# Performance work log

Measured on AMD Instinct MI355X. Metric: run time of the kernel, lower is better.

Reference implementation:

```python
import jax, jax.numpy as jnp
import numpy as np

D = 1024
H = 16
HD = D // H
SCALE = HD ** -0.5
EPS = 1e-5

def _ln(x, g, b):
    m = jnp.mean(x, axis=-1, keepdims=True)
    v = jnp.mean((x - m) ** 2, axis=-1, keepdims=True)
    return (x - m) / jnp.sqrt(v + EPS) * g + b

def setup_inputs() -> dict:
    key = jax.random.key(0)
    ks = jax.random.split(key, 16)
    B, Lq, Lk = 8, 1024, 1024
    s = 0.02
    inp = {
        "q": jax.random.normal(ks[0], (B, Lq, D), jnp.float32),
        "kv": jax.random.normal(ks[1], (B, Lk, D), jnp.float32),
        "kv_mask": jax.random.randint(ks[2], (B, Lk), 0, 2).astype(bool),
        "Wq": jax.random.normal(ks[3], (D, D), jnp.float32) * s,
        "bq": jnp.zeros((D,), jnp.float32),
        "Wk": jax.random.normal(ks[4], (D, D), jnp.float32) * s,
        "bk": jnp.zeros((D,), jnp.float32),
        "Wv": jax.random.normal(ks[5], (D, D), jnp.float32) * s,
        "bv": jnp.zeros((D,), jnp.float32),
        "Wo": jax.random.normal(ks[6], (D, D), jnp.float32) * s,
        "bo": jnp.zeros((D,), jnp.float32),
        "ln1_g": jnp.ones((D,), jnp.float32),
        "ln1_b": jnp.zeros((D,), jnp.float32),
        "W1": jax.random.normal(ks[7], (D, 4 * D), jnp.float32) * s,
        "b1": jnp.zeros((4 * D,), jnp.float32),
        "W2": jax.random.normal(ks[8], (4 * D, D), jnp.float32) * s,
        "b2": jnp.zeros((D,), jnp.float32),
        "ln2_g": jnp.ones((D,), jnp.float32),
        "ln2_b": jnp.zeros((D,), jnp.float32),
    }
    return inp

def reference(q, kv, kv_mask, Wq, bq, Wk, bk, Wv, bv, Wo, bo, ln1_g, ln1_b, W1, b1, W2, b2, ln2_g, ln2_b):
    B, Lq, _ = q.shape
    Lk = kv.shape[1]
    # projections -> [B, H, L, HD]
    qp = (q @ Wq + bq).reshape(B, Lq, H, HD).transpose(0, 2, 1, 3)
    kp = (kv @ Wk + bk).reshape(B, Lk, H, HD).transpose(0, 2, 1, 3)
    vp = (kv @ Wv + bv).reshape(B, Lk, H, HD).transpose(0, 2, 1, 3)
    scores = jnp.einsum('bhqd,bhkd->bhqk', qp, kp) * SCALE
    # mask: True = pad; if a row is all-pad, un-mask the last key position
    all_pad = jnp.all(kv_mask, axis=1)  # [B]
    mask = kv_mask.at[:, -1].set(jnp.where(all_pad, False, kv_mask[:, -1]))
    scores = jnp.where(mask[:, None, None, :], jnp.float32(-10000.0), scores)
    attn = jax.nn.softmax(scores, axis=-1)  # dropout is identity at eval
    out = jnp.einsum('bhqk,bhkd->bhqd', attn, vp)
    out = out.transpose(0, 2, 1, 3).reshape(B, Lq, D)
    out = out @ Wo + bo
    x = _ln(q + out, ln1_g, ln1_b)
    x2 = jax.nn.relu(x @ W1 + b1) @ W2 + b2
    return _ln(x + x2, ln2_g, ln2_b)
```

## Files before the change

### kernel.cpp

```cpp
#include <hip/hip_runtime.h>

typedef __bf16 bf16_t;
typedef bf16_t bf16x8 __attribute__((ext_vector_type(8)));
typedef bf16_t bf16x4 __attribute__((ext_vector_type(4)));
typedef float f32x4 __attribute__((ext_vector_type(4)));
typedef unsigned int u32;

typedef __attribute__((address_space(1))) unsigned as1_u32;
typedef __attribute__((address_space(3))) unsigned as3_u32;

#define LOG2E 1.4426950408889634f
#define QSCALE (0.125f * LOG2E)
#define MASK2 (-10000.0f * LOG2E)

__device__ __forceinline__ void gload16(const void* g, void* l) {
  __builtin_amdgcn_global_load_lds((as1_u32*)(void*)g, (as3_u32*)l, 16, 0, 0);
}

__global__ void cvt_qkv(const float* __restrict__ q, const float* __restrict__ kv,
                        bf16_t* __restrict__ qb, bf16_t* __restrict__ kvb) {
  long i = ((long)blockIdx.x * 256 + threadIdx.x) * 8;
  const float* src; bf16_t* dst;
  if (i < 8388608) { src = q + i; dst = qb + i; }
  else { src = kv + (i - 8388608); dst = kvb + (i - 8388608); }
  const float4 a = *(const float4*)src;
  const float4 b = *(const float4*)(src + 4);
  bf16x8 o;
  o[0] = (bf16_t)a.x; o[1] = (bf16_t)a.y; o[2] = (bf16_t)a.z; o[3] = (bf16_t)a.w;
  o[4] = (bf16_t)b.x; o[5] = (bf16_t)b.y; o[6] = (bf16_t)b.z; o[7] = (bf16_t)b.w;
  *(bf16x8*)dst = o;
}

__global__ void prep_mask(const unsigned char* __restrict__ mraw,
                          float* __restrict__ maskf) {
  __shared__ int sred[256];
  const int t = threadIdx.x, b = blockIdx.x;
  int f = 0;
  for (int i = t; i < 2048; i += 256) {
    u32 v = ((const u32*)mraw)[i];
    if (v & 0xFFFFFF00u) f = 1;
  }
  sred[t] = f; __syncthreads();
  for (int s = 128; s; s >>= 1) { if (t < s) sred[t] |= sred[t + s]; __syncthreads(); }
  const int isByte = sred[0];
  __syncthreads();

  int vals[4]; int allpad = 1;
#pragma unroll
  for (int i = 0; i < 4; i++) {
    int k = t * 4 + i;
    int mv = isByte ? (int)mraw[b * 1024 + k] : ((const int*)mraw)[b * 1024 + k];
    vals[i] = (mv != 0);
    allpad &= vals[i];
  }
  sred[t] = allpad; __syncthreads();
  for (int s = 128; s; s >>= 1) { if (t < s) sred[t] &= sred[t + s]; __syncthreads(); }
  const int ap = sred[0];
#pragma unroll
  for (int i = 0; i < 4; i++) {
    int k = t * 4 + i;
    int m = vals[i];
    if (ap && k == 1023) m = 0;
    maskf[b * 1024 + k] = m ? MASK2 : 0.0f;
  }
}

struct TP { const float* s; bf16_t* d; int K; int N; };
struct TP6 { TP t[6]; };
__global__ void transpose_all(TP6 args) {
  __shared__ float tile[64][65];
  int bid = blockIdx.x, z, tx, ty;
  if (bid < 1024)      { z = bid >> 8;  int r = bid & 255;  tx = r & 15; ty = r >> 4; }
  else if (bid < 2048) { z = 4;         int r = bid - 1024; tx = r & 63; ty = r >> 6; }
  else                 { z = 5;         int r = bid - 2048; tx = r & 15; ty = r >> 4; }
  const TP a = args.t[z];
  const int t = threadIdx.x;
  const int n0 = tx * 64, k0 = ty * 64;
#pragma unroll
  for (int i = 0; i < 16; i++) {
    int e = i * 256 + t; int r = e >> 6, c = e & 63;
    tile[r][c] = a.s[(size_t)(k0 + r) * a.N + n0 + c];
  }
  __syncthreads();
#pragma unroll
  for (int i = 0; i < 16; i++) {
    int e = i * 256 + t; int r = e >> 6, c = e & 63;
    a.d[(size_t)(n0 + r) * a.K + k0 + c] = (bf16_t)tile[c][r];
  }
}

template<int BM, int BN, int NT>
__global__ __launch_bounds__(NT, 2)
void gemm_bt(const bf16_t* __restrict__ A, const bf16_t* __restrict__ BT,
             const float* __restrict__ bias, bf16_t* __restrict__ C,
             int M, int N, int K, int relu, int bias_mode, float scale) {
  constexpr int WAVES = NT / 64;
  constexpr int WNC = (BN == 256) ? 4 : 2;
  constexpr int WMC = WAVES / WNC;
  constexpr int M_REP = BM / (WMC * 16);
  constexpr int N_REP = BN / (WNC * 16);
  constexpr int JA = BM * 8 / NT;
  constexpr int JB = BN * 8 / NT;

  __shared__ __align__(16) bf16_t As[2][BM * 64];
  __shared__ __align__(16) bf16_t Bs[2][BN * 64];

  const int tid = threadIdx.x;
  const int wave = tid >> 6, lane = tid & 63;
  const int quad = lane >> 4, l15 = lane & 15;
  const int gx = gridDim.x;
  const int nwg = gx * gridDim.y;
  int lin = blockIdx.y * gx + blockIdx.x;
  lin = (lin & 7) * (nwg >> 3) + (lin >> 3);
  const long bm = (long)(lin / gx) * BM, bn = (long)(lin % gx) * BN;
  const int wm = (wave / WNC) * (M_REP * 16), wn = (wave % WNC) * (N_REP * 16);

  const bf16_t* agp[JA];
  const bf16_t* bgp[JB];
#pragma unroll
  for (int j = 0; j < JA; j++) {
    int e = j * NT + tid, r = e >> 3, c = (e & 7) ^ (r & 7);
    agp[j] = A + (bm + r) * (long)K + c * 8;
  }
#pragma unroll
  for (int j = 0; j < JB; j++) {
    int e = j * NT + tid, r = e >> 3, c = (e & 7) ^ (r & 7);
    bgp[j] = BT + (bn + r) * (long)K + c * 8;
  }

  int aoff[M_REP][2], boff[N_REP][2];
#pragma unroll
  for (int mi = 0; mi < M_REP; mi++)
#pragma unroll
    for (int ks = 0; ks < 2; ks++) {
      int row = wm + mi * 16 + l15;
      aoff[mi][ks] = row * 64 + (((ks * 4 + quad) ^ (row & 7)) * 8);
    }
#pragma unroll
  for (int ni = 0; ni < N_REP; ni++)
#pragma unroll
    for (int ks = 0; ks < 2; ks++) {
      int row = wn + ni * 16 + l15;
      boff[ni][ks] = row * 64 + (((ks * 4 + quad) ^ (row & 7)) * 8);
    }

  f32x4 acc[M_REP][N_REP];
#pragma unroll
  for (int i = 0; i < M_REP; i++)
#pragma unroll
    for (int j = 0; j < N_REP; j++) acc[i][j] = (f32x4){0.f, 0.f, 0.f, 0.f};

  auto stage = [&](int kt, int s) {
#pragma unroll
    for (int j = 0; j < JA; j++)
      gload16(agp[j] + (long)kt * 64, &As[s][(j * NT + wave * 64) * 8]);
#pragma unroll
    for (int j = 0; j < JB; j++)
      gload16(bgp[j] + (long)kt * 64, &Bs[s][(j * NT + wave * 64) * 8]);
  };

  const int T = K >> 6;
  stage(0, 0);
  for (int t = 0; t < T; t++) {
    const int s = t & 1;
    if (t + 1 < T) {
      stage(t + 1, s ^ 1);
      asm volatile("s_waitcnt vmcnt(8)" ::: "memory");
    } else {
      asm volatile("s_waitcnt vmcnt(0)" ::: "memory");
    }
    __builtin_amdgcn_s_barrier();

#pragma unroll
    for (int ks = 0; ks < 2; ks++) {
      bf16x8 af[M_REP], bf[N_REP];
#pragma unroll
      for (int mi = 0; mi < M_REP; mi++) af[mi] = *(const bf16x8*)&As[s][aoff[mi][ks]];
#pragma unroll
      for (int ni = 0; ni < N_REP; ni++) bf[ni] = *(const bf16x8*)&Bs[s][boff[ni][ks]];
      __builtin_amdgcn_s_setprio(1);
#pragma unroll
      for (int mi = 0; mi < M_REP; mi++)
#pragma unroll
        for (int ni = 0; ni < N_REP; ni++)
          acc[mi][ni] = __builtin_amdgcn_mfma_f32_16x16x32_bf16(af[mi], bf[ni], acc[mi][ni], 0, 0, 0);
      __builtin_amdgcn_s_setprio(0);
    }
    asm volatile("s_waitcnt lgkmcnt(0)" ::: "memory");
    __builtin_amdgcn_s_barrier();
  }

#pragma unroll
  for (int mi = 0; mi < M_REP; mi++) {
#pragma unroll
    for (int ni = 0; ni < N_REP; ni++) {
      const long col = bn + wn + ni * 16 + l15;
      const float bc = bias_mode ? 0.f : bias[col];
#pragma unroll
      for (int r = 0; r < 4; r++) {
        const long row = bm + wm + mi * 16 + quad * 4 + r;
        const float bb = bias_mode ? bias[row] : bc;
        float v = (acc[mi][ni][r] + bb) * scale;
        if (relu) v = v > 0.f ? v : 0.f;
        C[row * N + col] = (bf16_t)v;
      }
    }
  }
}

__global__ __launch_bounds__(256, 4)
void attn(const bf16_t* __restrict__ Q, const bf16_t* __restrict__ Kp,
          const bf16_t* __restrict__ Vt, const float* __restrict__ maskf,
          bf16_t* __restrict__ AO) {
  __shared__ __align__(16) bf16_t Qs[64 * 64];
  __shared__ __align__(16) bf16_t Ks[64 * 64];
  __shared__ __align__(16) bf16_t Vts[64 * 64];
  __shared__ __align__(16) bf16_t Ps[4][16 * 64];
  __shared__ __align__(16) float msk[64];

  const int tid = threadIdx.x;
  const int wave = tid >> 6, lane = tid & 63;
  const int quad = lane >> 4, l15 = lane & 15;
  int lin = (blockIdx.z * 16 + blockIdx.y) * 16 + blockIdx.x;
  lin = (lin & 7) * 256 + (lin >> 3);
  const int q0 = (lin & 15) * 64;
  const int h = (lin >> 4) & 15;
  const int b = lin >> 8;

  const long base_q = ((long)b * 1024 + q0) * 1024 + h * 64;
  const long base_k = (long)b * 1024 * 1024 + h * 64;
  const long base_v = (long)h * 64 * 8192 + b * 1024;

  const int r0 = tid >> 3;
  const int c0 = ((tid & 7) ^ (r0 & 7)) * 8;
  const int r1 = (256 + tid) >> 3;
  const int c1 = (((256 + tid) & 7) ^ (r1 & 7)) * 8;
  const int wd0 = wave * 64 * 8;
  const int wd1 = (256 + wave * 64) * 8;

  const bf16_t* qg0 = Q + base_q + (long)r0 * 1024 + c0;
  const bf16_t* qg1 = Q + base_q + (long)r1 * 1024 + c1;
  const bf16_t* kg0 = Kp + base_k + (long)r0 * 1024 + c0;
  const bf16_t* kg1 = Kp + base_k + (long)r1 * 1024 + c1;
  const bf16_t* vg0 = Vt + base_v + (long)r0 * 8192 + c0;
  const bf16_t* vg1 = Vt + base_v + (long)r1 * 8192 + c1;
  const float* mrow = maskf + b * 1024;

  gload16(qg0, &Qs[wd0]);
  gload16(qg1, &Qs[wd1]);

  int offKV[4][2], offP[2], pwOff[4];
#pragma unroll
  for (int nt = 0; nt < 4; nt++)
#pragma unroll
    for (int ks = 0; ks < 2; ks++)
      offKV[nt][ks] = (nt * 16 + l15) * 64 + (((ks * 4 + quad) ^ (l15 & 7)) * 8);
#pragma unroll
  for (int ks = 0; ks < 2; ks++)
    offP[ks] = l15 * 64 + (((ks * 4 + quad) ^ (l15 & 7)) * 8);
#pragma unroll
  for (int nt = 0; nt < 4; nt++)
    pwOff[nt] = l15 * 64 + (((nt * 2 + (quad >> 1)) ^ (l15 & 7)) * 8) + (quad & 1) * 4;

  __syncthreads();

  bf16x8 aq[2];
#pragma unroll
  for (int ks = 0; ks < 2; ks++) {
    const int row = wave * 16 + l15;
    aq[ks] = *(const bf16x8*)&Qs[row * 64 + (((ks * 4 + quad) ^ (row & 7)) * 8)];
  }

  float m_i = -1e30f, l_i = 0.f;
  f32x4 o[4];
#pragma unroll
  for (int nt = 0; nt < 4; nt++) o[nt] = (f32x4){0.f, 0.f, 0.f, 0.f};

  bf16_t* Pw = &Ps[wave][0];

  for (int kt = 0; kt < 16; kt++) {
    const int k0 = kt * 64;
    __syncthreads();
    gload16(kg0 + (long)k0 * 1024, &Ks[wd0]);
    gload16(kg1 + (long)k0 * 1024, &Ks[wd1]);
    gload16(vg0 + k0, &Vts[wd0]);
    gload16(vg1 + k0, &Vts[wd1]);
    if (tid < 64) msk[tid] = mrow[k0 + tid];
    __syncthreads();

    f32x4 mv[4];
#pragma unroll
    for (int nt = 0; nt < 4; nt++)
      mv[nt] = *(const f32x4*)&msk[nt * 16 + quad * 4];

    f32x4 sc[4];
#pragma unroll
    for (int nt = 0; nt < 4; nt++) {
      f32x4 s = mv[nt];
#pragma unroll
      for (int ks = 0; ks < 2; ks++) {
        bf16x8 bk = *(const bf16x8*)&Ks[offKV[nt][ks]];
        s = __builtin_amdgcn_mfma_f32_16x16x32_bf16(bk, aq[ks], s, 0, 0, 0);
      }
      sc[nt] = s;
    }

    float mx = -1e30f;
#pragma unroll
    for (int nt = 0; nt < 4; nt++)
#pragma unroll
      for (int r = 0; r < 4; r++) mx = fmaxf(mx, sc[nt][r]);
    mx = fmaxf(mx, __shfl_xor(mx, 16));
    mx = fmaxf(mx, __shfl_xor(mx, 32));
    const float mnew = fmaxf(m_i, mx);
    const float alpha = exp2f(m_i - mnew);
    m_i = mnew;
    float ps = 0.f;
#pragma unroll
    for (int nt = 0; nt < 4; nt++)
#pragma unroll
      for (int r = 0; r < 4; r++) {
        const float p = exp2f(sc[nt][r] - mnew);
        sc[nt][r] = p;
        ps += p;
      }
    ps += __shfl_xor(ps, 16);
    ps += __shfl_xor(ps, 32);
    l_i = l_i * alpha + ps;

    float a4[4];
#pragma unroll
    for (int r = 0; r < 4; r++)
      a4[r] = __shfl(alpha, (quad << 4) | (quad * 4 + r));
#pragma unroll
    for (int nt = 0; nt < 4; nt++)
#pragma unroll
      for (int r = 0; r < 4; r++) o[nt][r] *= a4[r];

#pragma unroll
    for (int nt = 0; nt < 4; nt++) {
      bf16x4 pv;
#pragma unroll
      for (int r = 0; r < 4; r++) pv[r] = (bf16_t)sc[nt][r];
      *(bf16x4*)&Pw[pwOff[nt]] = pv;
    }

#pragma unroll
    for (int ks = 0; ks < 2; ks++) {
      bf16x8 ap = *(const bf16x8*)&Pw[offP[ks]];
#pragma unroll
      for (int nt = 0; nt < 4; nt++) {
        bf16x8 bv = *(const bf16x8*)&Vts[offKV[nt][ks]];
        o[nt] = __builtin_amdgcn_mfma_f32_16x16x32_bf16(ap, bv, o[nt], 0, 0, 0);
      }
    }
  }

  float linv[4];
#pragma unroll
  for (int r = 0; r < 4; r++)
    linv[r] = 1.0f / __shfl(l_i, (quad << 4) | (quad * 4 + r));
#pragma unroll
  for (int r = 0; r < 4; r++) {
    const int row = q0 + wave * 16 + quad * 4 + r;
#pragma unroll
    for (int nt = 0; nt < 4; nt++) {
      const int col = h * 64 + nt * 16 + l15;
      AO[((long)b * 1024 + row) * 1024 + col] = (bf16_t)(o[nt][r] * linv[r]);
    }
  }
}

__global__ __launch_bounds__(256)
void ln_res1(const float* __restrict__ xa, const bf16_t* __restrict__ xb,
             const float* __restrict__ g, const float* __restrict__ bt,
             bf16_t* __restrict__ out) {
  __shared__ float sw[8];
  const int t = threadIdx.x, w = t >> 6;
  const long row = blockIdx.x;
  const float4 a = *(const float4*)(xa + row * 1024 + t * 4);
  const bf16x4 bq = *(const bf16x4*)(xb + row * 1024 + t * 4);
  float v[4] = {a.x + (float)bq[0], a.y + (float)bq[1],
                a.z + (float)bq[2], a.w + (float)bq[3]};
  float s = v[0] + v[1] + v[2] + v[3];
  float s2 = v[0]*v[0] + v[1]*v[1] + v[2]*v[2] + v[3]*v[3];
#pragma unroll
  for (int off = 1; off < 64; off <<= 1) {
    s += __shfl_xor(s, off); s2 += __shfl_xor(s2, off);
  }
  if ((t & 63) == 0) { sw[w] = s; sw[4 + w] = s2; }
  __syncthreads();
  s = sw[0] + sw[1] + sw[2] + sw[3];
  s2 = sw[4] + sw[5] + sw[6] + sw[7];
  const float mean = s * (1.f / 1024.f);
  const float var = s2 * (1.f / 1024.f) - mean * mean;
  const float rstd = rsqrtf(var + 1e-5f);
  bf16x4 o;
#pragma unroll
  for (int i = 0; i < 4; i++) {
    const int c = t * 4 + i;
    o[i] = (bf16_t)((v[i] - mean) * rstd * g[c] + bt[c]);
  }
  *(bf16x4*)(out + row * 1024 + t * 4) = o;
}

__global__ __launch_bounds__(256)
void ln_res2(const bf16_t* __restrict__ xa, const bf16_t* __restrict__ xb,
             const float* __restrict__ g, const float* __restrict__ bt,
             float* __restrict__ out) {
  __shared__ float sw[8];
  const int t = threadIdx.x, w = t >> 6;
  const long row = blockIdx.x;
  const bf16x4 aq = *(const bf16x4*)(xa + row * 1024 + t * 4);
  const bf16x4 bq = *(const bf16x4*)(xb + row * 1024 + t * 4);
  float v[4];
#pragma unroll
  for (int i = 0; i < 4; i++) v[i] = (float)aq[i] + (float)bq[i];
  float s = v[0] + v[1] + v[2] + v[3];
  float s2 = v[0]*v[0] + v[1]*v[1] + v[2]*v[2] + v[3]*v[3];
#pragma unroll
  for (int off = 1; off < 64; off <<= 1) {
    s += __shfl_xor(s, off); s2 += __shfl_xor(s2, off);
  }
  if ((t & 63) == 0) { sw[w] = s; sw[4 + w] = s2; }
  __syncthreads();
  s = sw[0] + sw[1] + sw[2] + sw[3];
  s2 = sw[4] + sw[5] + sw[6] + sw[7];
  const float mean = s * (1.f / 1024.f);
  const float var = s2 * (1.f / 1024.f) - mean * mean;
  const float rstd = rsqrtf(var + 1e-5f);
  float4 o;
  o.x = (v[0] - mean) * rstd * g[t*4+0] + bt[t*4+0];
  o.y = (v[1] - mean) * rstd * g[t*4+1] + bt[t*4+1];
  o.z = (v[2] - mean) * rstd * g[t*4+2] + bt[t*4+2];
  o.w = (v[3] - mean) * rstd * g[t*4+3] + bt[t*4+3];
  *(float4*)(out + row * 1024 + t * 4) = o;
}

extern "C" void kernel_launch(void* const* d_in, const int* in_sizes, int n_in,
                              void* d_out, int out_size, void* d_ws, size_t ws_size,
                              hipStream_t stream) {
  (void)in_sizes; (void)n_in; (void)out_size; (void)ws_size;
  const float* q   = (const float*)d_in[0];
  const float* kv  = (const float*)d_in[1];
  const unsigned char* mraw = (const unsigned char*)d_in[2];
  const float* Wq = (const float*)d_in[3];
  const float* bq = (const float*)d_in[4];
  const float* Wk = (const float*)d_in[5];
  const float* bk = (const float*)d_in[6];
  const float* Wv = (const float*)d_in[7];
  const float* bv = (const float*)d_in[8];
  const float* Wo = (const float*)d_in[9];
  const float* bo = (const float*)d_in[10];
  const float* g1 = (const float*)d_in[11];
  const float* be1 = (const float*)d_in[12];
  const float* W1 = (const float*)d_in[13];
  const float* b1 = (const float*)d_in[14];
  const float* W2 = (const float*)d_in[15];
  const float* b2 = (const float*)d_in[16];
  const float* g2 = (const float*)d_in[17];
  const float* be2 = (const float*)d_in[18];
  float* out = (float*)d_out;

  char* ws = (char*)d_ws;
  size_t off = 0;
  auto alloc = [&](size_t bytes) -> char* {
    char* p = ws + off; off += (bytes + 255) & ~(size_t)255; return p;
  };
  const size_t MB16 = (size_t)8192 * 1024 * 2;
  float*  maskf = (float*)alloc(8192 * 4);
  bf16_t* WqT = (bf16_t*)alloc((size_t)1024 * 1024 * 2);
  bf16_t* WkT = (bf16_t*)alloc((size_t)1024 * 1024 * 2);
  bf16_t* WvT = (bf16_t*)alloc((size_t)1024 * 1024 * 2);
  bf16_t* WoT = (bf16_t*)alloc((size_t)1024 * 1024 * 2);
  bf16_t* W1T = (bf16_t*)alloc((size_t)1024 * 4096 * 2);
  bf16_t* W2T = (bf16_t*)alloc((size_t)4096 * 1024 * 2);
  bf16_t* Qp = (bf16_t*)alloc(MB16);
  bf16_t* Kp = (bf16_t*)alloc(MB16);
  bf16_t* VT = (bf16_t*)alloc(MB16);
  bf16_t* AO = (bf16_t*)alloc(MB16);
  bf16_t* X1 = (bf16_t*)alloc(MB16);
  bf16_t* TL = (bf16_t*)alloc(MB16);
  bf16_t* qb  = X1;
  bf16_t* kvb = TL;
  bf16_t* HF  = Qp;
  bf16_t* OP  = Kp;
  bf16_t* F2  = WqT;

  cvt_qkv<<<8192, 256, 0, stream>>>(q, kv, qb, kvb);
  prep_mask<<<8, 256, 0, stream>>>(mraw, maskf);
  TP6 tp = {{ {Wq, WqT, 1024, 1024}, {Wk, WkT, 1024, 1024},
              {Wv, WvT, 1024, 1024}, {Wo, WoT, 1024, 1024},
              {W1, W1T, 1024, 4096}, {W2, W2T, 4096, 1024} }};
  transpose_all<<<3072, 256, 0, stream>>>(tp);

  const dim3 gproj(8, 64);
  gemm_bt<128,128,256><<<gproj, 256, 0, stream>>>(qb,  WqT, bq, Qp, 8192, 1024, 1024, 0, 0, QSCALE);
  gemm_bt<128,128,256><<<gproj, 256, 0, stream>>>(kvb, WkT, bk, Kp, 8192, 1024, 1024, 0, 0, 1.f);
  gemm_bt<128,128,256><<<dim3(64, 8), 256, 0, stream>>>(WvT, kvb, bv, VT, 1024, 8192, 1024, 0, 1, 1.f);

  attn<<<dim3(16, 16, 8), 256, 0, stream>>>(Qp, Kp, VT, maskf, AO);

  gemm_bt<128,128,256><<<gproj, 256, 0, stream>>>(AO, WoT, bo, OP, 8192, 1024, 1024, 0, 0, 1.f);
  ln_res1<<<8192, 256, 0, stream>>>(q, OP, g1, be1, X1);

  gemm_bt<256,256,512><<<dim3(16, 32), 512, 0, stream>>>(X1, W1T, b1, HF, 8192, 4096, 1024, 1, 0, 1.f);
  gemm_bt<128,128,256><<<gproj, 256, 0, stream>>>(HF, W2T, b2, F2, 8192, 1024, 4096, 0, 0, 1.f);
  ln_res2<<<8192, 256, 0, stream>>>(X1, F2, g2, be2, out);
}
```

Measured before the change: 556.7 us.

## Add ping-pong pipelined 256x256 GEMM kernel for the FFN up-projection

Adds a dedicated 512-thread GEMM kernel for the W1 projection. It uses double-buffered LDS with global_load_lds and issues the next tile's loads in four chunks interleaved between MFMA phases, with barriers and s_setprio to overlap memory with compute. It also remaps workgroup IDs across groups of eight for better L2 locality and uses XOR-swizzled LDS offsets. The extra barriers and the large accumulator register footprint at 8x4 tiles per wave could limit occupancy.

Result: no change. 549.9 us (-1.2%).

```diff
diff --git a/kernel.cpp b/kernel.cpp
--- a/kernel.cpp
+++ b/kernel.cpp
@@ -201,6 +201,118 @@
         const long row = bm + wm + mi * 16 + quad * 4 + r;
         const float bb = bias_mode ? bias[row] : bc;
         float v = (acc[mi][ni][r] + bb) * scale;
+        if (relu) v = v > 0.f ? v : 0.f;
+        C[row * N + col] = (bf16_t)v;
+      }
+    }
+  }
+}
+
+__global__ __launch_bounds__(512, 2)
+void gemm_8p(const bf16_t* __restrict__ A, const bf16_t* __restrict__ BT,
+             const float* __restrict__ bias, bf16_t* __restrict__ C,
+             int M, int N, int K, int relu, float scale) {
+  __shared__ __align__(16) bf16_t As[2][256 * 64];
+  __shared__ __align__(16) bf16_t Bs[2][256 * 64];
+
+  const int tid = threadIdx.x;
+  const int wave = tid >> 6, lane = tid & 63;
+  const int quad = lane >> 4, l15 = lane & 15;
+  const int gx = gridDim.x;
+  const int nwg = gx * gridDim.y;
+  int lin = blockIdx.y * gx + blockIdx.x;
+  lin = (lin & 7) * (nwg >> 3) + (lin >> 3);
+  const long bm = (long)(lin / gx) * 256, bn = (long)(lin % gx) * 256;
+  const int wm = (wave >> 2) * 128, wn = (wave & 3) * 64;
+
+  const int r_ = tid >> 3;
+  const int cs_ = ((tid & 7) ^ (r_ & 7)) * 8;
+  const bf16_t* ag = A + (bm + r_) * (long)K + cs_;
+  const bf16_t* bg = BT + (bn + r_) * (long)K + cs_;
+
+  int aoff[8][2], boff[4][2];
+#pragma unroll
+  for (int mi = 0; mi < 8; mi++)
+#pragma unroll
+    for (int ks = 0; ks < 2; ks++) {
+      int row = wm + mi * 16 + l15;
+      aoff[mi][ks] = row * 64 + (((ks * 4 + quad) ^ (row & 7)) * 8);
+    }
+#pragma unroll
+  for (int ni = 0; ni < 4; ni++)
+#pragma unroll
+    for (int ks = 0; ks < 2; ks++) {
+      int row = wn + ni * 16 + l15;
+      boff[ni][ks] = row * 64 + (((ks * 4 + quad) ^ (row & 7)) * 8);
+    }
+
+  f32x4 acc[8][4];
+#pragma unroll
+  for (int i = 0; i < 8; i++)
+#pragma unroll
+    for (int j = 0; j < 4; j++) acc[i][j] = (f32x4){0.f, 0.f, 0.f, 0.f};
+
+  auto stagePair = [&](int kt, int s, int j) {
+    gload16(ag + (long)(j * 64) * K + (long)kt * 64, &As[s][(j * 512 + wave * 64) * 8]);
+    gload16(bg + (long)(j * 64) * K + (long)kt * 64, &Bs[s][(j * 512 + wave * 64) * 8]);
+  };
+
+  const int T = K >> 6;
+#pragma unroll
+  for (int j = 0; j < 4; j++) stagePair(0, 0, j);
+
+#pragma unroll 1
+  for (int t = 0; t < T; t++) {
+    const int s = t & 1;
+    if (t + 1 < T) {
+      stagePair(t + 1, s ^ 1, 0);
+      asm volatile("s_waitcnt vmcnt(2)" ::: "memory");
+    } else {
+      asm volatile("s_waitcnt vmcnt(0)" ::: "memory");
+    }
+    __builtin_amdgcn_s_barrier();
+
+    bf16x8 bf[4][2];
+#pragma unroll
+    for (int ni = 0; ni < 4; ni++)
+#pragma unroll
+      for (int ks = 0; ks < 2; ks++)
+        bf[ni][ks] = *(const bf16x8*)&Bs[s][boff[ni][ks]];
+
+#pragma unroll
+    for (int p = 0; p < 4; p++) {
+      bf16x8 af[2][2];
+#pragma unroll
+      for (int i = 0; i < 2; i++)
+#pragma unroll
+        for (int ks = 0; ks < 2; ks++)
+          af[i][ks] = *(const bf16x8*)&As[s][aoff[p * 2 + i][ks]];
+      if (p < 3 && t + 1 < T) stagePair(t + 1, s ^ 1, p + 1);
+      __builtin_amdgcn_s_barrier();
+      __builtin_amdgcn_s_setprio(1);
+#pragma unroll
+      for (int i = 0; i < 2; i++)
+#pragma unroll
+        for (int ni = 0; ni < 4; ni++)
+#pragma unroll
+          for (int ks = 0; ks < 2; ks++)
+            acc[p * 2 + i][ni] = __builtin_amdgcn_mfma_f32_16x16x32_bf16(
+                af[i][ks], bf[ni][ks], acc[p * 2 + i][ni], 0, 0, 0);
+      __builtin_amdgcn_s_setprio(0);
+      __builtin_amdgcn_s_barrier();
+    }
+  }
+
+#pragma unroll
+  for (int mi = 0; mi < 8; mi++) {
+#pragma unroll
+    for (int ni = 0; ni < 4; ni++) {
+      const long col = bn + wn + ni * 16 + l15;
+      const float bc = bias[col];
+#pragma unroll
+      for (int r = 0; r < 4; r++) {
+        const long row = bm + wm + mi * 16 + quad * 4 + r;
+        float v = (acc[mi][ni][r] + bc) * scale;
         if (relu) v = v > 0.f ? v : 0.f;
         C[row * N + col] = (bf16_t)v;
       }
@@ -504,7 +616,7 @@
   gemm_bt<128,128,256><<<gproj, 256, 0, stream>>>(AO, WoT, bo, OP, 8192, 1024, 1024, 0, 0, 1.f);
   ln_res1<<<8192, 256, 0, stream>>>(q, OP, g1, be1, X1);
 
-  gemm_bt<256,256,512><<<dim3(16, 32), 512, 0, stream>>>(X1, W1T, b1, HF, 8192, 4096, 1024, 1, 0, 1.f);
+  gemm_8p<<<dim3(16, 32), 512, 0, stream>>>(X1, W1T, b1, HF, 8192, 4096, 1024, 1, 1.f);
   gemm_bt<128,128,256><<<gproj, 256, 0, stream>>>(HF, W2T, b2, F2, 8192, 1024, 4096, 0, 0, 1.f);
   ln_res2<<<8192, 256, 0, stream>>>(X1, F2, g2, be2, out);
 }
```
